# Optimization experiments

Measured on AMD Instinct MI355X. Metric: run time of the kernel, lower is better.

## Reference

```python
import jax, jax.numpy as jnp
import numpy as np

N, E, NODE_DIM, EDGE_DIM, H, L, G, C = 50000, 600000, 64, 16, 128, 3, 256, 2


def setup_inputs() -> dict:
    key = jax.random.key(0)
    ks = jax.random.split(key, 32)
    inp = {
        "x": jax.random.normal(ks[0], (N, NODE_DIM), jnp.float32),
        "edge_attr": jax.random.normal(ks[1], (E, EDGE_DIM), jnp.float32),
        "edge_index": jax.random.randint(ks[2], (2, E), 0, N, dtype=jnp.int64),
        "batch": jnp.sort(jax.random.randint(ks[3], (N,), 0, G, dtype=jnp.int64)),
    }
    def lin(k, fan_in, fan_out):
        b = 1.0 / np.sqrt(fan_in)
        return jax.random.uniform(k, (fan_in, fan_out), jnp.float32, -b, b)
    # node embedding
    inp["emb_W"] = lin(ks[4], NODE_DIM, H)
    inp["emb_b"] = jnp.zeros((H,), jnp.float32)
    # stacked per-layer MPNN params [L, ...]
    inp["msg_W1"] = jnp.stack([lin(jax.random.fold_in(ks[5], i), 2 * H + EDGE_DIM, H) for i in range(L)])
    inp["msg_b1"] = jnp.zeros((L, H), jnp.float32)
    inp["msg_W2"] = jnp.stack([lin(jax.random.fold_in(ks[6], i), H, H) for i in range(L)])
    inp["msg_b2"] = jnp.zeros((L, H), jnp.float32)
    inp["upd_W1"] = jnp.stack([lin(jax.random.fold_in(ks[7], i), 2 * H, H) for i in range(L)])
    inp["upd_b1"] = jnp.zeros((L, H), jnp.float32)
    inp["upd_W2"] = jnp.stack([lin(jax.random.fold_in(ks[8], i), H, H) for i in range(L)])
    inp["upd_b2"] = jnp.zeros((L, H), jnp.float32)
    # classifier (dropout is eval-mode identity)
    inp["cls_W1"] = lin(ks[9], 2 * H, H)
    inp["cls_b1"] = jnp.zeros((H,), jnp.float32)
    inp["cls_W2"] = lin(ks[10], H, H // 2)
    inp["cls_b2"] = jnp.zeros((H // 2,), jnp.float32)
    inp["cls_W3"] = lin(ks[11], H // 2, C)
    inp["cls_b3"] = jnp.zeros((C,), jnp.float32)
    return inp


def reference(x, edge_attr, emb_W, emb_b, msg_W1, msg_b1, msg_W2, msg_b2,
              upd_W1, upd_b1, upd_W2, upd_b2,
              cls_W1, cls_b1, cls_W2, cls_b2, cls_W3, cls_b3,
              edge_index, batch):
    src, dst = edge_index[0], edge_index[1]  # PyG: x_j = x[src], x_i = x[dst]
    h = x @ emb_W + emb_b  # [N, H]
    for l in range(L):
        x_i = h[dst]
        x_j = h[src]
        msg_in = jnp.concatenate([x_i, x_j, edge_attr], axis=1)  # [E, 2H+edge_dim]
        m = jax.nn.relu(msg_in @ msg_W1[l] + msg_b1[l]) @ msg_W2[l] + msg_b2[l]
        aggr = jax.ops.segment_sum(m, dst, num_segments=N)  # scatter-add to targets
        upd_in = jnp.concatenate([h, aggr], axis=1)  # [N, 2H]
        h = jax.nn.relu(upd_in @ upd_W1[l] + upd_b1[l]) @ upd_W2[l] + upd_b2[l]
        h = jax.nn.relu(h)
    # global mean / max pool over graphs
    counts = jax.ops.segment_sum(jnp.ones((N,), h.dtype), batch, num_segments=G)
    g_mean = jax.ops.segment_sum(h, batch, num_segments=G) / jnp.maximum(counts, 1.0)[:, None]
    g_max = jax.ops.segment_max(h, batch, num_segments=G)
    g_max = jnp.where(jnp.isfinite(g_max), g_max, 0.0)  # guard empty graphs
    rep = jnp.concatenate([g_mean, g_max], axis=1)  # [G, 2H]
    # classifier (dropout = identity in eval)
    z = jax.nn.relu(rep @ cls_W1 + cls_b1)
    z = jax.nn.relu(z @ cls_W2 + cls_b2)
    return z @ cls_W3 + cls_b3  # [G, C]
```

## Files before the change

### kernel.cpp

```cpp
#include <hip/hip_runtime.h>
#include <hip/hip_bf16.h>

#define HD 128
#define SCB 2048

typedef __attribute__((ext_vector_type(8))) short short8v;
typedef __attribute__((ext_vector_type(4))) float f32x4;
typedef unsigned short us;

__device__ __forceinline__ us f2bf(float f) {
    union { float f; unsigned u; } c; c.f = f;
    unsigned u = c.u;
    return (us)((u + 0x7fffu + ((u >> 16) & 1u)) >> 16);
}
__device__ __forceinline__ float bf2f(us b) {
    union { unsigned u; float f; } c; c.u = ((unsigned)b) << 16;
    return c.f;
}

__device__ __forceinline__ void gload16(const void* g, void* l) {
    __builtin_amdgcn_global_load_lds(
        (const __attribute__((address_space(1))) unsigned int*)g,
        (__attribute__((address_space(3))) unsigned int*)l,
        16, 0, 0);
}

template<int KSTEPS, int K1S, bool HASA2, bool RELU, bool DEGB, bool WF32, bool WBF>
__global__ __launch_bounds__(512) void k_mgemm(
    const us* __restrict__ A1h, const us* __restrict__ A1l,
    const us* __restrict__ A2h, const us* __restrict__ A2l,
    const us* __restrict__ Wth, const us* __restrict__ Wtl,
    const float* __restrict__ bias,
    const float* __restrict__ bdeg, const float* __restrict__ deg,
    float* __restrict__ Cf0, float* __restrict__ Cf1,
    us* __restrict__ Ch, us* __restrict__ Cl,
    int nrows)
{
    constexpr int K   = KSTEPS * 32;
    constexpr int CPR = K / 8;
    constexpr int ITER = (64 * CPR) / 512;
    __shared__ us As_h[64 * K];
    __shared__ us As_l[64 * K];

    const int tid  = threadIdx.x;
    const int wv   = tid >> 6;
    const int lane = tid & 63;
    const int r    = lane & 15;
    const int g    = lane >> 4;
    const int rb   = blockIdx.x * 64;
    const int col  = blockIdx.y * 128 + wv * 16 + r;

    short8v bh[KSTEPS], bl[KSTEPS];
    {
        size_t wbase = (size_t)col * K + (size_t)(g * 8);
#pragma unroll
        for (int s = 0; s < KSTEPS; ++s) {
            bh[s] = *(const short8v*)(Wth + wbase + s * 32);
            bl[s] = *(const short8v*)(Wtl + wbase + s * 32);
        }
    }

#pragma unroll
    for (int i = 0; i < ITER; ++i) {
        int f = tid + i * 512;
        int row = f / CPR, c = f % CPR;
        int grow = rb + row; if (grow >= nrows) grow = nrows - 1;
        int sb = (c * 16) ^ ((row & 7) << 4);
        const char *gh, *gl;
        if (!HASA2 || sb < K1S * 2) {
            gh = (const char*)A1h + (size_t)grow * (K1S * 2) + sb;
            gl = (const char*)A1l + (size_t)grow * (K1S * 2) + sb;
        } else {
            gh = (const char*)A2h + (size_t)grow * ((K - K1S) * 2) + (sb - K1S * 2);
            gl = (const char*)A2l + (size_t)grow * ((K - K1S) * 2) + (sb - K1S * 2);
        }
        gload16(gh, (char*)As_h + (size_t)f * 16);
        gload16(gl, (char*)As_l + (size_t)f * 16);
    }
    __syncthreads();

    f32x4 acc[4];
#pragma unroll
    for (int t = 0; t < 4; ++t) acc[t] = (f32x4){0.f, 0.f, 0.f, 0.f};

#pragma unroll
    for (int s = 0; s < KSTEPS; ++s) {
#pragma unroll
        for (int t = 0; t < 4; ++t) {
            int row = t * 16 + r;
            int boff = row * (K * 2) + (((s * 64) + g * 16) ^ ((row & 7) << 4));
            short8v ah = *(const short8v*)((const char*)As_h + boff);
            short8v al = *(const short8v*)((const char*)As_l + boff);
            acc[t] = __builtin_amdgcn_mfma_f32_16x16x32_bf16(ah, bh[s], acc[t], 0, 0, 0);
            acc[t] = __builtin_amdgcn_mfma_f32_16x16x32_bf16(al, bh[s], acc[t], 0, 0, 0);
            acc[t] = __builtin_amdgcn_mfma_f32_16x16x32_bf16(ah, bl[s], acc[t], 0, 0, 0);
        }
    }

    const float bb = (bias && col < 128) ? bias[col] : 0.f;
    const float bd = (DEGB && col < 128) ? bdeg[col] : 0.f;
    const int jc = col & 127;
#pragma unroll
    for (int t = 0; t < 4; ++t) {
#pragma unroll
        for (int i = 0; i < 4; ++i) {
            int row = rb + t * 16 + g * 4 + i;
            if (row >= nrows) continue;
            float v = acc[t][i] + bb;
            if (DEGB) v += deg[row] * bd;
            if (RELU) v = fmaxf(v, 0.f);
            size_t o = (size_t)row * HD + jc;
            if (WF32) (col < 128 ? Cf0 : Cf1)[o] = v;
            if (WBF) {
                us hh = f2bf(v);
                Ch[o] = hh;
                Cl[o] = f2bf(v - bf2f(hh));
            }
        }
    }
}

__global__ __launch_bounds__(512) void k_upd(
    const us* __restrict__ A1h, const us* __restrict__ A1l,
    const us* __restrict__ A2h, const us* __restrict__ A2l,
    const us* __restrict__ Wth, const us* __restrict__ Wtl,
    const float* __restrict__ b1,
    const float* __restrict__ bdeg, const float* __restrict__ deg,
    const us* __restrict__ W2th, const us* __restrict__ W2tl,
    const float* __restrict__ b2,
    us* __restrict__ out_h, us* __restrict__ out_l,
    int nrows)
{
    constexpr int K = 256;
    constexpr int CPR = K / 8;
    constexpr int ITER = (64 * CPR) / 512;
    __shared__ us As_h[64 * K];
    __shared__ us As_l[64 * K];

    const int tid  = threadIdx.x;
    const int wv   = tid >> 6;
    const int lane = tid & 63;
    const int r    = lane & 15;
    const int g    = lane >> 4;
    const int rb   = blockIdx.x * 64;
    const int col  = wv * 16 + r;

    short8v bh[8], bl[8];
    {
        size_t wbase = (size_t)col * K + (size_t)(g * 8);
#pragma unroll
        for (int s = 0; s < 8; ++s) {
            bh[s] = *(const short8v*)(Wth + wbase + s * 32);
            bl[s] = *(const short8v*)(Wtl + wbase + s * 32);
        }
    }

#pragma unroll
    for (int i = 0; i < ITER; ++i) {
        int f = tid + i * 512;
        int row = f / CPR, c = f % CPR;
        int grow = rb + row; if (grow >= nrows) grow = nrows - 1;
        int sb = (c * 16) ^ ((row & 7) << 4);
        const char *gh, *gl;
        if (sb < 256) {
            gh = (const char*)A1h + (size_t)grow * 256 + sb;
            gl = (const char*)A1l + (size_t)grow * 256 + sb;
        } else {
            gh = (const char*)A2h + (size_t)grow * 256 + (sb - 256);
            gl = (const char*)A2l + (size_t)grow * 256 + (sb - 256);
        }
        gload16(gh, (char*)As_h + (size_t)f * 16);
        gload16(gl, (char*)As_l + (size_t)f * 16);
    }
    __syncthreads();

    f32x4 acc[4];
#pragma unroll
    for (int t = 0; t < 4; ++t) acc[t] = (f32x4){0.f, 0.f, 0.f, 0.f};
#pragma unroll
    for (int s = 0; s < 8; ++s) {
#pragma unroll
        for (int t = 0; t < 4; ++t) {
            int row = t * 16 + r;
            int boff = row * (K * 2) + (((s * 64) + g * 16) ^ ((row & 7) << 4));
            short8v ah = *(const short8v*)((const char*)As_h + boff);
            short8v al = *(const short8v*)((const char*)As_l + boff);
            acc[t] = __builtin_amdgcn_mfma_f32_16x16x32_bf16(ah, bh[s], acc[t], 0, 0, 0);
            acc[t] = __builtin_amdgcn_mfma_f32_16x16x32_bf16(al, bh[s], acc[t], 0, 0, 0);
            acc[t] = __builtin_amdgcn_mfma_f32_16x16x32_bf16(ah, bl[s], acc[t], 0, 0, 0);
        }
    }
    __syncthreads();

    short8v b2h[4], b2l[4];
    {
        size_t wbase = (size_t)col * 128 + (size_t)(g * 8);
#pragma unroll
        for (int s = 0; s < 4; ++s) {
            b2h[s] = *(const short8v*)(W2th + wbase + s * 32);
            b2l[s] = *(const short8v*)(W2tl + wbase + s * 32);
        }
    }

    {
        const float bb = b1[col];
        const float bd = bdeg[col];
#pragma unroll
        for (int t = 0; t < 4; ++t) {
#pragma unroll
            for (int i = 0; i < 4; ++i) {
                int lrow = t * 16 + g * 4 + i;
                int grow = rb + lrow;
                float dg = (grow < nrows) ? deg[grow] : 0.f;
                float v = acc[t][i] + bb + dg * bd;
                v = fmaxf(v, 0.f);
                us uh = f2bf(v);
                us ul = f2bf(v - bf2f(uh));
                int byte = lrow * 256 + ((col * 2) ^ ((lrow & 7) << 4));
                *(us*)((char*)As_h + byte) = uh;
                *(us*)((char*)As_l + byte) = ul;
            }
        }
    }
    __syncthreads();

    f32x4 acc2[4];
#pragma unroll
    for (int t = 0; t < 4; ++t) acc2[t] = (f32x4){0.f, 0.f, 0.f, 0.f};
#pragma unroll
    for (int s = 0; s < 4; ++s) {
#pragma unroll
        for (int t = 0; t < 4; ++t) {
            int row = t * 16 + r;
            int boff = row * 256 + (((s * 64) + g * 16) ^ ((row & 7) << 4));
            short8v ah = *(const short8v*)((const char*)As_h + boff);
            short8v al = *(const short8v*)((const char*)As_l + boff);
            acc2[t] = __builtin_amdgcn_mfma_f32_16x16x32_bf16(ah, b2h[s], acc2[t], 0, 0, 0);
            acc2[t] = __builtin_amdgcn_mfma_f32_16x16x32_bf16(al, b2h[s], acc2[t], 0, 0, 0);
            acc2[t] = __builtin_amdgcn_mfma_f32_16x16x32_bf16(ah, b2l[s], acc2[t], 0, 0, 0);
        }
    }
    const float bb2 = b2[col];
#pragma unroll
    for (int t = 0; t < 4; ++t) {
#pragma unroll
        for (int i = 0; i < 4; ++i) {
            int row = rb + t * 16 + g * 4 + i;
            if (row >= nrows) continue;
            float v = fmaxf(acc2[t][i] + bb2, 0.f);
            size_t o = (size_t)row * HD + col;
            us hh = f2bf(v);
            out_h[o] = hh;
            out_l[o] = f2bf(v - bf2f(hh));
        }
    }
}

__global__ void k_cvtA(const float* __restrict__ src,
                       us* __restrict__ dh, us* __restrict__ dl, long n)
{
    long i = (long)blockIdx.x * blockDim.x + threadIdx.x;
    if (i >= n) return;
    float v = src[i];
    us h = f2bf(v);
    dh[i] = h;
    dl[i] = f2bf(v - bf2f(h));
}

__global__ void k_cvtW(const float* __restrict__ src, long sstride, int K,
                       us* __restrict__ dh, us* __restrict__ dl, long dstride)
{
    int l = blockIdx.y;
    int idx = blockIdx.x * 256 + threadIdx.x;
    if (idx >= K * 128) return;
    int k = idx >> 7, j = idx & 127;
    float v = src[(size_t)l * sstride + (size_t)k * 128 + j];
    us h = f2bf(v);
    size_t o = (size_t)l * dstride + (size_t)j * K + k;
    dh[o] = h;
    dl[o] = f2bf(v - bf2f(h));
}

__global__ void k_cvtW2(const float* __restrict__ srcA, long strideA,
                        const float* __restrict__ srcB, long strideB,
                        int K1s, int K,
                        us* __restrict__ dh, us* __restrict__ dl, long dstride)
{
    int l = blockIdx.y;
    int idx = blockIdx.x * 256 + threadIdx.x;
    if (idx >= K * 128) return;
    int k = idx >> 7, j = idx & 127;
    float v = (k < K1s)
        ? srcA[(size_t)l * strideA + (size_t)k * 128 + j]
        : srcB[(size_t)l * strideB + (size_t)(k - K1s) * 128 + j];
    us h = f2bf(v);
    size_t o = (size_t)l * dstride + (size_t)j * K + k;
    dh[o] = h;
    dl[o] = f2bf(v - bf2f(h));
}

__global__ void k_deghist(const int* __restrict__ dst, int* __restrict__ degi, int E,
                          const int* __restrict__ batch, int* __restrict__ gcnt, int N)
{
    int i = blockIdx.x * blockDim.x + threadIdx.x;
    if (i < E) atomicAdd(&degi[dst[i]], 1);
    if (i < N) atomicAdd(&gcnt[batch[i]], 1);
}

__global__ __launch_bounds__(256) void k_scan1(const int* __restrict__ degi,
                                               int* __restrict__ thrpre,
                                               int* __restrict__ bsum, int N)
{
    __shared__ int sc[256];
    const int t = threadIdx.x, b = blockIdx.x;
    int i0 = b * SCB + t * 8;
    int s = 0;
#pragma unroll
    for (int q = 0; q < 8; ++q) {
        int i = i0 + q;
        if (i < N) s += degi[i];
    }
    sc[t] = s;
    __syncthreads();
    for (int o = 1; o < 256; o <<= 1) {
        int v = (t >= o) ? sc[t - o] : 0;
        __syncthreads();
        sc[t] += v;
        __syncthreads();
    }
    thrpre[b * 256 + t] = sc[t] - s;
    if (t == 255) bsum[b] = sc[255];
}

__global__ void k_scan2(const int* __restrict__ bsum, int* __restrict__ boff, int nb)
{
    if (threadIdx.x == 0 && blockIdx.x == 0) {
        int run = 0;
        for (int b = 0; b < nb; ++b) { boff[b] = run; run += bsum[b]; }
    }
}

__global__ __launch_bounds__(256) void k_scan3(
    const int* __restrict__ degi, const int* __restrict__ thrpre,
    const int* __restrict__ boff,
    int* __restrict__ rowptr, int* __restrict__ cursor,
    float* __restrict__ degf, int N, int E)
{
    const int t = threadIdx.x, b = blockIdx.x;
    int run = boff[b] + thrpre[b * 256 + t];
    int i0 = b * SCB + t * 8;
#pragma unroll
    for (int q = 0; q < 8; ++q) {
        int i = i0 + q;
        if (i < N) {
            int d = degi[i];
            rowptr[i] = run;
            cursor[i] = run;
            degf[i] = (float)d;
            run += d;
        }
    }
    if (b == 0 && t == 0) rowptr[N] = E;
}

__global__ void k_scatter(const int* __restrict__ dst, const int* __restrict__ src,
                          int* __restrict__ cursor,
                          const float* __restrict__ ea,
                          int* __restrict__ csr_src, int* __restrict__ csr_eid,
                          float* __restrict__ ea_p, int E)
{
    int e = blockIdx.x * blockDim.x + threadIdx.x;
    if (e >= E) return;
    int d = dst[e];
    int pos = atomicAdd(&cursor[d], 1);
    csr_src[pos] = src[e];
    if (ea_p) {
        const float4* s4 = (const float4*)&ea[(size_t)e * 16];
        float4* d4 = (float4*)&ea_p[(size_t)pos * 16];
        d4[0] = s4[0]; d4[1] = s4[1]; d4[2] = s4[2]; d4[3] = s4[3];
    } else {
        csr_eid[pos] = e;
    }
}

__global__ __launch_bounds__(256) void k_foldW(
    const float* __restrict__ msg_W2, const float* __restrict__ upd_W1,
    float* __restrict__ fold)
{
    int l = blockIdx.x >> 3, rb = blockIdx.x & 7;
    const float* W2  = msg_W2 + (size_t)l * HD * HD;
    const float* U1b = upd_W1 + (size_t)l * 256 * HD + (size_t)HD * HD;
    float* Wout = fold + (size_t)l * HD * HD;
    int j = threadIdx.x & 127;
    int rh = threadIdx.x >> 7;
    int r0 = rb * 16 + rh * 8;
    float acc[8] = {0.f,0.f,0.f,0.f,0.f,0.f,0.f,0.f};
    for (int k = 0; k < HD; ++k) {
        float u = U1b[(size_t)k * HD + j];
#pragma unroll
        for (int rr = 0; rr < 8; ++rr)
            acc[rr] = fmaf(W2[(size_t)(r0 + rr) * HD + k], u, acc[rr]);
    }
#pragma unroll
    for (int rr = 0; rr < 8; ++rr)
        Wout[(size_t)(r0 + rr) * HD + j] = acc[rr];
}

__global__ __launch_bounds__(128) void k_foldb(
    const float* __restrict__ msg_b2, const float* __restrict__ upd_W1,
    float* __restrict__ bvec2)
{
    int l = blockIdx.x, j = threadIdx.x;
    const float* U1b = upd_W1 + (size_t)l * 256 * HD + (size_t)HD * HD;
    const float* b2 = msg_b2 + (size_t)l * HD;
    float acc = 0.f;
    for (int k = 0; k < HD; ++k) acc = fmaf(b2[k], U1b[(size_t)k * HD + j], acc);
    bvec2[(size_t)l * HD + j] = acc;
}

#define EB 16
template<bool PERM>
__global__ __launch_bounds__(256) void k_edge(
    const float* __restrict__ P, const float* __restrict__ Q,
    const float* __restrict__ EA,
    const int* __restrict__ rowptr,
    const int* __restrict__ csr_src, const int* __restrict__ csr_eid,
    const float* __restrict__ W1c,
    us* __restrict__ Sh, us* __restrict__ Sl, int N)
{
    const int lane = threadIdx.x & 63;
    const int node = __builtin_amdgcn_readfirstlane(blockIdx.x * 4 + (threadIdx.x >> 6));
    if (node >= N) return;
    float wA[16], wB[16];
#pragma unroll
    for (int k = 0; k < 16; ++k) {
        wA[k] = W1c[k * HD + lane];
        wB[k] = W1c[k * HD + 64 + lane];
    }
    const int beg = __builtin_amdgcn_readfirstlane(rowptr[node]);
    const int end = __builtin_amdgcn_readfirstlane(rowptr[node + 1]);
    const float pA = P[(size_t)node * HD + lane];
    const float pB = P[(size_t)node * HD + 64 + lane];
    float accA = 0.f, accB = 0.f;

    for (int i = beg; i < end; i += EB) {
        int myi = i + (lane & 15);
        myi = (myi < end) ? myi : (end - 1);
        int myidx = PERM ? myi : csr_eid[myi];
        int mysrc = csr_src[myi];
        int sv[EB], ei[EB];
#pragma unroll
        for (int r = 0; r < EB; ++r) {
            sv[r] = __builtin_amdgcn_readlane(mysrc, r);
            ei[r] = PERM ? 0 : __builtin_amdgcn_readlane(myidx, r);
        }
        float qA[EB], qB[EB];
#pragma unroll
        for (int r = 0; r < EB; ++r) {
            qA[r] = Q[(size_t)sv[r] * HD + lane];
            qB[r] = Q[(size_t)sv[r] * HD + 64 + lane];
        }
#pragma unroll
        for (int r = 0; r < EB; ++r) {
            int ii = i + r; ii = (ii < end) ? ii : (end - 1);
            const float4* Ev = PERM ? (const float4*)&EA[(size_t)ii * 16]
                                    : (const float4*)&EA[(size_t)ei[r] * 16];
            float4 v0 = Ev[0], v1 = Ev[1], v2 = Ev[2], v3 = Ev[3];
            float tA = pA + qA[r], tB = pB + qB[r];
            tA = fmaf(v0.x, wA[0],  tA); tB = fmaf(v0.x, wB[0],  tB);
            tA = fmaf(v0.y, wA[1],  tA); tB = fmaf(v0.y, wB[1],  tB);
            tA = fmaf(v0.z, wA[2],  tA); tB = fmaf(v0.z, wB[2],  tB);
            tA = fmaf(v0.w, wA[3],  tA); tB = fmaf(v0.w, wB[3],  tB);
            tA = fmaf(v1.x, wA[4],  tA); tB = fmaf(v1.x, wB[4],  tB);
            tA = fmaf(v1.y, wA[5],  tA); tB = fmaf(v1.y, wB[5],  tB);
            tA = fmaf(v1.z, wA[6],  tA); tB = fmaf(v1.z, wB[6],  tB);
            tA = fmaf(v1.w, wA[7],  tA); tB = fmaf(v1.w, wB[7],  tB);
            tA = fmaf(v2.x, wA[8],  tA); tB = fmaf(v2.x, wB[8],  tB);
            tA = fmaf(v2.y, wA[9],  tA); tB = fmaf(v2.y, wB[9],  tB);
            tA = fmaf(v2.z, wA[10], tA); tB = fmaf(v2.z, wB[10], tB);
            tA = fmaf(v2.w, wA[11], tA); tB = fmaf(v2.w, wB[11], tB);
            tA = fmaf(v3.x, wA[12], tA); tB = fmaf(v3.x, wB[12], tB);
            tA = fmaf(v3.y, wA[13], tA); tB = fmaf(v3.y, wB[13], tB);
            tA = fmaf(v3.z, wA[14], tA); tB = fmaf(v3.z, wB[14], tB);
            tA = fmaf(v3.w, wA[15], tA); tB = fmaf(v3.w, wB[15], tB);
            bool ok = (i + r) < end;
            accA += ok ? fmaxf(tA, 0.f) : 0.f;
            accB += ok ? fmaxf(tB, 0.f) : 0.f;
        }
    }
    size_t oA = (size_t)node * HD + lane;
    size_t oB = oA + 64;
    us hA = f2bf(accA);
    us hB = f2bf(accB);
    Sh[oA] = hA; Sl[oA] = f2bf(accA - bf2f(hA));
    Sh[oB] = hB; Sl[oB] = f2bf(accB - bf2f(hB));
}

__global__ __launch_bounds__(256) void k_pool2(
    const us* __restrict__ hh, const us* __restrict__ hl,
    const int* __restrict__ batch,
    float* __restrict__ gsum, unsigned int* __restrict__ gmax, int N)
{
    int nchunk = (N + gridDim.x - 1) / gridDim.x;
    int n0 = blockIdx.x * nchunk;
    int n1 = n0 + nchunk; if (n1 > N) n1 = N;
    int j = threadIdx.x & 127;
    int half = threadIdx.x >> 7;
    float s = 0.f, m = 0.f; int gcur = -1;
    for (int n = n0 + half; n < n1; n += 2) {
        int g = batch[n];
        if (g != gcur) {
            if (gcur >= 0) {
                atomicAdd(&gsum[(size_t)gcur * HD + j], s);
                atomicMax(&gmax[(size_t)gcur * HD + j], __float_as_uint(m));
            }
            gcur = g; s = 0.f; m = 0.f;
        }
        size_t o = (size_t)n * HD + j;
        float v = bf2f(hh[o]) + bf2f(hl[o]);
        s += v; m = fmaxf(m, v);
    }
    if (gcur >= 0) {
        atomicAdd(&gsum[(size_t)gcur * HD + j], s);
        atomicMax(&gmax[(size_t)gcur * HD + j], __float_as_uint(m));
    }
}

__global__ __launch_bounds__(128) void k_cls(
    const float* __restrict__ gsum, const float* __restrict__ gmax,
    const int* __restrict__ gcnt,
    const float* __restrict__ W1, const float* __restrict__ b1,
    const float* __restrict__ W2, const float* __restrict__ b2,
    const float* __restrict__ W3, const float* __restrict__ b3,
    float* __restrict__ out)
{
    __shared__ float rep[256];
    __shared__ float z1[128];
    __shared__ float z2[64];
    const int g = blockIdx.x;
    const int j = threadIdx.x;
    float cntf = (float)gcnt[g];
    rep[j]       = gsum[(size_t)g * HD + j] / fmaxf(cntf, 1.f);
    rep[128 + j] = gmax[(size_t)g * HD + j];
    __syncthreads();
    float a = 0.f;
    for (int k = 0; k < 256; ++k) a = fmaf(rep[k], W1[(size_t)k * 128 + j], a);
    z1[j] = fmaxf(a + b1[j], 0.f);
    __syncthreads();
    if (j < 64) {
        float b = 0.f;
        for (int k = 0; k < 128; ++k) b = fmaf(z1[k], W2[(size_t)k * 64 + j], b);
        z2[j] = fmaxf(b + b2[j], 0.f);
    }
    __syncthreads();
    if (j < 2) {
        float c = 0.f;
        for (int k = 0; k < 64; ++k) c = fmaf(z2[k], W3[(size_t)k * 2 + j], c);
        out[(size_t)g * 2 + j] = c + b3[j];
    }
}

extern "C" void kernel_launch(void* const* d_in, const int* in_sizes, int n_in,
                              void* d_out, int out_size, void* d_ws, size_t ws_size,
                              hipStream_t stream) {
    const float* x      = (const float*)d_in[0];
    const float* ea     = (const float*)d_in[1];
    const int*   ei     = (const int*)d_in[2];
    const int*   batch  = (const int*)d_in[3];
    const float* emb_W  = (const float*)d_in[4];
    const float* emb_b  = (const float*)d_in[5];
    const float* msg_W1 = (const float*)d_in[6];
    const float* msg_b1 = (const float*)d_in[7];
    const float* msg_W2 = (const float*)d_in[8];
    const float* msg_b2 = (const float*)d_in[9];
    const float* upd_W1 = (const float*)d_in[10];
    const float* upd_b1 = (const float*)d_in[11];
    const float* upd_W2 = (const float*)d_in[12];
    const float* upd_b2 = (const float*)d_in[13];
    const float* cW1 = (const float*)d_in[14];
    const float* cb1 = (const float*)d_in[15];
    const float* cW2 = (const float*)d_in[16];
    const float* cb2 = (const float*)d_in[17];
    const float* cW3 = (const float*)d_in[18];
    const float* cb3 = (const float*)d_in[19];

    const int N = in_sizes[0] / 64;
    const int E = in_sizes[1] / 16;
    const int G = 256, L = 3;
    const int* src = ei;
    const int* dst = ei + E;
    const int nb = (N + SCB - 1) / SCB;

    char* w = (char*)d_ws;
    size_t off = 0;
    auto alloc = [&](size_t bytes) -> void* {
        void* p = w + off;
        off += (bytes + 255) & ~(size_t)255;
        return p;
    };
    float* Pb  = (float*)alloc((size_t)N * HD * 4);
    float* Qb  = (float*)alloc((size_t)N * HD * 4);
    us* S_h = (us*)alloc((size_t)N * HD * 2);
    us* S_l = (us*)alloc((size_t)N * HD * 2);
    us* h_h = (us*)alloc((size_t)N * HD * 2);
    us* h_l = (us*)alloc((size_t)N * HD * 2);
    us* x_h = S_h;
    us* x_l = S_l;
    float* fold  = (float*)alloc((size_t)L * HD * HD * 4);
    float* bvec2 = (float*)alloc((size_t)L * HD * 4);
    us* embt_h = (us*)alloc((size_t)128 * 64 * 2);
    us* embt_l = (us*)alloc((size_t)128 * 64 * 2);
    us* WPQt_h = (us*)alloc((size_t)L * 256 * 128 * 2);
    us* WPQt_l = (us*)alloc((size_t)L * 256 * 128 * 2);
    us* Wcbt_h = (us*)alloc((size_t)L * 128 * 256 * 2);
    us* Wcbt_l = (us*)alloc((size_t)L * 128 * 256 * 2);
    us* U2t_h  = (us*)alloc((size_t)L * 128 * 128 * 2);
    us* U2t_l  = (us*)alloc((size_t)L * 128 * 128 * 2);
    int*   degi   = (int*)alloc((size_t)N * 4);
    float* degf   = (float*)alloc((size_t)N * 4);
    int*   rowptr = (int*)alloc((size_t)(N + 1) * 4);
    int*   cursor = (int*)alloc((size_t)N * 4);
    int*   thrpre = (int*)alloc((size_t)nb * 256 * 4);
    int*   bsum   = (int*)alloc((size_t)(nb + 1) * 4);
    int*   boff   = (int*)alloc((size_t)(nb + 1) * 4);
    int*   gcnt   = (int*)alloc(256 * 4);
    float* gsum   = (float*)alloc((size_t)G * HD * 4);
    float* gmax   = (float*)alloc((size_t)G * HD * 4);
    int*   csr_src = (int*)alloc((size_t)E * 4);
    int*   csr_eid = (int*)alloc((size_t)E * 4);
    float* ea_p = nullptr;
    if (ws_size && off + (size_t)E * 16 * 4 + 256 <= ws_size)
        ea_p = (float*)alloc((size_t)E * 16 * 4);
    (void)n_in; (void)out_size;

    hipMemsetAsync(degi, 0, (size_t)N * 4, stream);
    hipMemsetAsync(gcnt, 0, 256 * 4, stream);
    hipMemsetAsync(gsum, 0, (size_t)G * HD * 4, stream);
    hipMemsetAsync(gmax, 0, (size_t)G * HD * 4, stream);

    int mEN = (E > N ? E : N);
    k_deghist<<<(mEN + 255) / 256, 256, 0, stream>>>(dst, degi, E, batch, gcnt, N);
    k_scan1<<<nb, 256, 0, stream>>>(degi, thrpre, bsum, N);
    k_scan2<<<1, 64, 0, stream>>>(bsum, boff, nb);
    k_scan3<<<nb, 256, 0, stream>>>(degi, thrpre, boff, rowptr, cursor, degf, N, E);
    k_scatter<<<(E + 255) / 256, 256, 0, stream>>>(dst, src, cursor, ea,
                                                   csr_src, csr_eid, ea_p, E);

    k_foldW<<<L * 8, 256, 0, stream>>>(msg_W2, upd_W1, fold);
    k_foldb<<<L, 128, 0, stream>>>(msg_b2, upd_W1, bvec2);

    k_cvtA<<<(int)(((long)N * 64 + 255) / 256), 256, 0, stream>>>(x, x_h, x_l, (long)N * 64);
    k_cvtW<<<dim3(32, 1), 256, 0, stream>>>(emb_W, 0, 64, embt_h, embt_l, 0);
    k_cvtW<<<dim3(64, L), 256, 0, stream>>>(msg_W1, 272 * 128, 128,
                                            WPQt_h, WPQt_l, 256 * 128);
    k_cvtW<<<dim3(64, L), 256, 0, stream>>>(msg_W1 + 128 * 128, 272 * 128, 128,
                                            WPQt_h + 128 * 128, WPQt_l + 128 * 128,
                                            256 * 128);
    k_cvtW2<<<dim3(128, L), 256, 0, stream>>>(upd_W1, 256 * 128, fold, 128 * 128,
                                              128, 256, Wcbt_h, Wcbt_l, 128 * 256);
    k_cvtW<<<dim3(64, L), 256, 0, stream>>>(upd_W2, 128 * 128, 128,
                                            U2t_h, U2t_l, 128 * 128);

    const int gb = (N + 63) / 64;
    k_mgemm<2, 64, false, false, false, false, true><<<dim3(gb, 1), 512, 0, stream>>>(
        x_h, x_l, nullptr, nullptr, embt_h, embt_l,
        emb_b, nullptr, nullptr, nullptr, nullptr, h_h, h_l, N);

    for (int l = 0; l < L; ++l) {
        const float* W1 = msg_W1 + (size_t)l * 272 * HD;
        k_mgemm<4, 128, false, false, false, true, false><<<dim3(gb, 2), 512, 0, stream>>>(
            h_h, h_l, nullptr, nullptr,
            WPQt_h + (size_t)l * 256 * 128, WPQt_l + (size_t)l * 256 * 128,
            msg_b1 + (size_t)l * HD, nullptr, nullptr, Pb, Qb, nullptr, nullptr, N);
        if (ea_p)
            k_edge<true><<<(N + 3) / 4, 256, 0, stream>>>(Pb, Qb, ea_p, rowptr,
                                                          csr_src, nullptr,
                                                          W1 + 256 * HD, S_h, S_l, N);
        else
            k_edge<false><<<(N + 3) / 4, 256, 0, stream>>>(Pb, Qb, ea, rowptr,
                                                           csr_src, csr_eid,
                                                           W1 + 256 * HD, S_h, S_l, N);
        k_upd<<<gb, 512, 0, stream>>>(
            h_h, h_l, S_h, S_l,
            Wcbt_h + (size_t)l * 128 * 256, Wcbt_l + (size_t)l * 128 * 256,
            upd_b1 + (size_t)l * HD, bvec2 + (size_t)l * HD, degf,
            U2t_h + (size_t)l * 128 * 128, U2t_l + (size_t)l * 128 * 128,
            upd_b2 + (size_t)l * HD,
            h_h, h_l, N);
    }

    k_pool2<<<1024, 256, 0, stream>>>(h_h, h_l, batch, gsum, (unsigned int*)gmax, N);
    k_cls<<<G, 128, 0, stream>>>(gsum, gmax, gcnt, cW1, cb1, cW2, cb2, cW3, cb3,
                                 (float*)d_out);
}
```

Before: 685.5 us.

## Fuse per-layer P/Q projection GEMM into embedding and update kernels

The standalone per-layer GEMM that computes the P and Q node projections is removed. That projection now runs inside the embedding kernel for layer 0 and inside the update kernel for the following layer. The freshly computed h tile is written back to shared memory and immediately multiplied by the W_P/W_Q weights, so h is not re-read from global memory and launches are saved. In exchange, the fused kernels use more registers for the extra weight fragments and accumulators, which may reduce occupancy.

```diff
diff --git a/kernel.cpp b/kernel.cpp
--- a/kernel.cpp
+++ b/kernel.cpp
@@ -25,22 +25,17 @@
         16, 0, 0);
 }
 
-template<int KSTEPS, int K1S, bool HASA2, bool RELU, bool DEGB, bool WF32, bool WBF>
-__global__ __launch_bounds__(512) void k_mgemm(
-    const us* __restrict__ A1h, const us* __restrict__ A1l,
-    const us* __restrict__ A2h, const us* __restrict__ A2l,
-    const us* __restrict__ Wth, const us* __restrict__ Wtl,
-    const float* __restrict__ bias,
-    const float* __restrict__ bdeg, const float* __restrict__ deg,
-    float* __restrict__ Cf0, float* __restrict__ Cf1,
-    us* __restrict__ Ch, us* __restrict__ Cl,
-    int nrows)
-{
-    constexpr int K   = KSTEPS * 32;
-    constexpr int CPR = K / 8;
-    constexpr int ITER = (64 * CPR) / 512;
-    __shared__ us As_h[64 * K];
-    __shared__ us As_l[64 * K];
+__global__ __launch_bounds__(512) void k_embpq(
+    const us* __restrict__ xh, const us* __restrict__ xl,
+    const us* __restrict__ embth, const us* __restrict__ embtl,
+    const float* __restrict__ emb_b,
+    const us* __restrict__ wpqh, const us* __restrict__ wpql,
+    const float* __restrict__ b1msg,
+    us* __restrict__ out_h, us* __restrict__ out_l,
+    float* __restrict__ Pb, float* __restrict__ Qb, int nrows)
+{
+    __shared__ us As_h[8192];
+    __shared__ us As_l[8192];
 
     const int tid  = threadIdx.x;
     const int wv   = tid >> 6;
@@ -48,47 +43,37 @@
     const int r    = lane & 15;
     const int g    = lane >> 4;
     const int rb   = blockIdx.x * 64;
-    const int col  = blockIdx.y * 128 + wv * 16 + r;
-
-    short8v bh[KSTEPS], bl[KSTEPS];
-    {
-        size_t wbase = (size_t)col * K + (size_t)(g * 8);
-#pragma unroll
-        for (int s = 0; s < KSTEPS; ++s) {
-            bh[s] = *(const short8v*)(Wth + wbase + s * 32);
-            bl[s] = *(const short8v*)(Wtl + wbase + s * 32);
-        }
-    }
-
-#pragma unroll
-    for (int i = 0; i < ITER; ++i) {
-        int f = tid + i * 512;
-        int row = f / CPR, c = f % CPR;
+    const int col  = wv * 16 + r;
+
+    short8v bh[2], bl[2];
+    {
+        size_t wbase = (size_t)col * 64 + (size_t)(g * 8);
+#pragma unroll
+        for (int s = 0; s < 2; ++s) {
+            bh[s] = *(const short8v*)(embth + wbase + s * 32);
+            bl[s] = *(const short8v*)(embtl + wbase + s * 32);
+        }
+    }
+
+    {
+        int f = tid;
+        int row = f >> 3, c = f & 7;
         int grow = rb + row; if (grow >= nrows) grow = nrows - 1;
         int sb = (c * 16) ^ ((row & 7) << 4);
-        const char *gh, *gl;
-        if (!HASA2 || sb < K1S * 2) {
-            gh = (const char*)A1h + (size_t)grow * (K1S * 2) + sb;
-            gl = (const char*)A1l + (size_t)grow * (K1S * 2) + sb;
-        } else {
-            gh = (const char*)A2h + (size_t)grow * ((K - K1S) * 2) + (sb - K1S * 2);
-            gl = (const char*)A2l + (size_t)grow * ((K - K1S) * 2) + (sb - K1S * 2);
-        }
-        gload16(gh, (char*)As_h + (size_t)f * 16);
-        gload16(gl, (char*)As_l + (size_t)f * 16);
+        gload16((const char*)xh + (size_t)grow * 128 + sb, (char*)As_h + (size_t)f * 16);
+        gload16((const char*)xl + (size_t)grow * 128 + sb, (char*)As_l + (size_t)f * 16);
     }
     __syncthreads();
 
     f32x4 acc[4];
 #pragma unroll
     for (int t = 0; t < 4; ++t) acc[t] = (f32x4){0.f, 0.f, 0.f, 0.f};
-
-#pragma unroll
-    for (int s = 0; s < KSTEPS; ++s) {
+#pragma unroll
+    for (int s = 0; s < 2; ++s) {
 #pragma unroll
         for (int t = 0; t < 4; ++t) {
             int row = t * 16 + r;
-            int boff = row * (K * 2) + (((s * 64) + g * 16) ^ ((row & 7) << 4));
+            int boff = row * 128 + (((s * 64) + g * 16) ^ ((row & 7) << 4));
             short8v ah = *(const short8v*)((const char*)As_h + boff);
             short8v al = *(const short8v*)((const char*)As_l + boff);
             acc[t] = __builtin_amdgcn_mfma_f32_16x16x32_bf16(ah, bh[s], acc[t], 0, 0, 0);
@@ -96,31 +81,84 @@
             acc[t] = __builtin_amdgcn_mfma_f32_16x16x32_bf16(ah, bl[s], acc[t], 0, 0, 0);
         }
     }
-
-    const float bb = (bias && col < 128) ? bias[col] : 0.f;
-    const float bd = (DEGB && col < 128) ? bdeg[col] : 0.f;
-    const int jc = col & 127;
+    __syncthreads();
+
+    {
+        const float bbE = emb_b[col];
+#pragma unroll
+        for (int t = 0; t < 4; ++t) {
+#pragma unroll
+            for (int i = 0; i < 4; ++i) {
+                int lrow = t * 16 + g * 4 + i;
+                int grow = rb + lrow;
+                float v = acc[t][i] + bbE;
+                us hh = f2bf(v);
+                us hl2 = f2bf(v - bf2f(hh));
+                if (grow < nrows) {
+                    size_t o = (size_t)grow * HD + col;
+                    out_h[o] = hh; out_l[o] = hl2;
+                }
+                int byte = lrow * 256 + ((col * 2) ^ ((lrow & 7) << 4));
+                *(us*)((char*)As_h + byte) = hh;
+                *(us*)((char*)As_l + byte) = hl2;
+            }
+        }
+    }
+    __syncthreads();
+
+    short8v bPh[4], bPl[4], bQh[4], bQl[4];
+    {
+        size_t baseP = (size_t)col * 128 + (size_t)(g * 8);
+        size_t baseQ = (size_t)(col + 128) * 128 + (size_t)(g * 8);
+#pragma unroll
+        for (int s = 0; s < 4; ++s) {
+            bPh[s] = *(const short8v*)(wpqh + baseP + s * 32);
+            bPl[s] = *(const short8v*)(wpql + baseP + s * 32);
+            bQh[s] = *(const short8v*)(wpqh + baseQ + s * 32);
+            bQl[s] = *(const short8v*)(wpql + baseQ + s * 32);
+        }
+    }
+
+    f32x4 accP[4], accQ[4];
 #pragma unroll
     for (int t = 0; t < 4; ++t) {
-#pragma unroll
-        for (int i = 0; i < 4; ++i) {
-            int row = rb + t * 16 + g * 4 + i;
-            if (row >= nrows) continue;
-            float v = acc[t][i] + bb;
-            if (DEGB) v += deg[row] * bd;
-            if (RELU) v = fmaxf(v, 0.f);
-            size_t o = (size_t)row * HD + jc;
-            if (WF32) (col < 128 ? Cf0 : Cf1)[o] = v;
-            if (WBF) {
-                us hh = f2bf(v);
-                Ch[o] = hh;
-                Cl[o] = f2bf(v - bf2f(hh));
+        accP[t] = (f32x4){0.f, 0.f, 0.f, 0.f};
+        accQ[t] = (f32x4){0.f, 0.f, 0.f, 0.f};
+    }
+#pragma unroll
+    for (int s = 0; s < 4; ++s) {
+#pragma unroll
+        for (int t = 0; t < 4; ++t) {
+            int row = t * 16 + r;
+            int boff = row * 256 + (((s * 64) + g * 16) ^ ((row & 7) << 4));
+            short8v ah = *(const short8v*)((const char*)As_h + boff);
+            short8v al = *(const short8v*)((const char*)As_l + boff);
+            accP[t] = __builtin_amdgcn_mfma_f32_16x16x32_bf16(ah, bPh[s], accP[t], 0, 0, 0);
+            accP[t] = __builtin_amdgcn_mfma_f32_16x16x32_bf16(al, bPh[s], accP[t], 0, 0, 0);
+            accP[t] = __builtin_amdgcn_mfma_f32_16x16x32_bf16(ah, bPl[s], accP[t], 0, 0, 0);
+            accQ[t] = __builtin_amdgcn_mfma_f32_16x16x32_bf16(ah, bQh[s], accQ[t], 0, 0, 0);
+            accQ[t] = __builtin_amdgcn_mfma_f32_16x16x32_bf16(al, bQh[s], accQ[t], 0, 0, 0);
+            accQ[t] = __builtin_amdgcn_mfma_f32_16x16x32_bf16(ah, bQl[s], accQ[t], 0, 0, 0);
+        }
+    }
+    {
+        const float bbP = b1msg[col];
+#pragma unroll
+        for (int t = 0; t < 4; ++t) {
+#pragma unroll
+            for (int i = 0; i < 4; ++i) {
+                int row = rb + t * 16 + g * 4 + i;
+                if (row >= nrows) continue;
+                size_t o = (size_t)row * HD + col;
+                Pb[o] = accP[t][i] + bbP;
+                Qb[o] = accQ[t][i];
             }
         }
     }
 }
 
-__global__ __launch_bounds__(512) void k_upd(
+template<bool DOPQ>
+__global__ __launch_bounds__(512) void k_updpq(
     const us* __restrict__ A1h, const us* __restrict__ A1l,
     const us* __restrict__ A2h, const us* __restrict__ A2l,
     const us* __restrict__ Wth, const us* __restrict__ Wtl,
@@ -128,7 +166,10 @@
     const float* __restrict__ bdeg, const float* __restrict__ deg,
     const us* __restrict__ W2th, const us* __restrict__ W2tl,
     const float* __restrict__ b2,
+    const us* __restrict__ wpqh, const us* __restrict__ wpql,
+    const float* __restrict__ b1msg,
     us* __restrict__ out_h, us* __restrict__ out_l,
+    float* __restrict__ Pb, float* __restrict__ Qb,
     int nrows)
 {
     constexpr int K = 256;
@@ -240,18 +281,94 @@
             acc2[t] = __builtin_amdgcn_mfma_f32_16x16x32_bf16(ah, b2l[s], acc2[t], 0, 0, 0);
         }
     }
-    const float bb2 = b2[col];
+    if (!DOPQ) {
+        const float bb2 = b2[col];
+#pragma unroll
+        for (int t = 0; t < 4; ++t) {
+#pragma unroll
+            for (int i = 0; i < 4; ++i) {
+                int row = rb + t * 16 + g * 4 + i;
+                if (row >= nrows) continue;
+                float v = fmaxf(acc2[t][i] + bb2, 0.f);
+                size_t o = (size_t)row * HD + col;
+                us hh = f2bf(v);
+                out_h[o] = hh;
+                out_l[o] = f2bf(v - bf2f(hh));
+            }
+        }
+        return;
+    }
+
+    __syncthreads();
+    {
+        const float bb2 = b2[col];
+#pragma unroll
+        for (int t = 0; t < 4; ++t) {
+#pragma unroll
+            for (int i = 0; i < 4; ++i) {
+                int lrow = t * 16 + g * 4 + i;
+                int grow = rb + lrow;
+                float v = fmaxf(acc2[t][i] + bb2, 0.f);
+                us hh = f2bf(v);
+                us hl2 = f2bf(v - bf2f(hh));
+                if (grow < nrows) {
+                    size_t o = (size_t)grow * HD + col;
+                    out_h[o] = hh; out_l[o] = hl2;
+                }
+                int byte = lrow * 256 + ((col * 2) ^ ((lrow & 7) << 4));
+                *(us*)((char*)As_h + byte) = hh;
+                *(us*)((char*)As_l + byte) = hl2;
+            }
+        }
+    }
+    __syncthreads();
+
+    short8v bPh[4], bPl[4], bQh[4], bQl[4];
+    {
+        size_t baseP = (size_t)col * 128 + (size_t)(g * 8);
+        size_t baseQ = (size_t)(col + 128) * 128 + (size_t)(g * 8);
+#pragma unroll
+        for (int s = 0; s < 4; ++s) {
+            bPh[s] = *(const short8v*)(wpqh + baseP + s * 32);
+            bPl[s] = *(const short8v*)(wpql + baseP + s * 32);
+            bQh[s] = *(const short8v*)(wpqh + baseQ + s * 32);
+            bQl[s] = *(const short8v*)(wpql + baseQ + s * 32);
+        }
+    }
+    f32x4 accP[4], accQ[4];
 #pragma unroll
     for (int t = 0; t < 4; ++t) {
-#pragma unroll
-        for (int i = 0; i < 4; ++i) {
-            int row = rb + t * 16 + g * 4 + i;
-            if (row >= nrows) continue;
-            float v = fmaxf(acc2[t][i] + bb2, 0.f);
-            size_t o = (size_t)row * HD + col;
-            us hh = f2bf(v);
-            out_h[o] = hh;
-            out_l[o] = f2bf(v - bf2f(hh));
+        accP[t] = (f32x4){0.f, 0.f, 0.f, 0.f};
+        accQ[t] = (f32x4){0.f, 0.f, 0.f, 0.f};
+    }
+#pragma unroll
+    for (int s = 0; s < 4; ++s) {
+#pragma unroll
+        for (int t = 0; t < 4; ++t) {
+            int row = t * 16 + r;
+            int boff = row * 256 + (((s * 64) + g * 16) ^ ((row & 7) << 4));
+            short8v ah = *(const short8v*)((const char*)As_h + boff);
+            short8v al = *(const short8v*)((const char*)As_l + boff);
+            accP[t] = __builtin_amdgcn_mfma_f32_16x16x32_bf16(ah, bPh[s], accP[t], 0, 0, 0);
+            accP[t] = __builtin_amdgcn_mfma_f32_16x16x32_bf16(al, bPh[s], accP[t], 0, 0, 0);
+            accP[t] = __builtin_amdgcn_mfma_f32_16x16x32_bf16(ah, bPl[s], accP[t], 0, 0, 0);
+            accQ[t] = __builtin_amdgcn_mfma_f32_16x16x32_bf16(ah, bQh[s], accQ[t], 0, 0, 0);
+            accQ[t] = __builtin_amdgcn_mfma_f32_16x16x32_bf16(al, bQh[s], accQ[t], 0, 0, 0);
+            accQ[t] = __builtin_amdgcn_mfma_f32_16x16x32_bf16(ah, bQl[s], accQ[t], 0, 0, 0);
+        }
+    }
+    {
+        const float bbP = b1msg[col];
+#pragma unroll
+        for (int t = 0; t < 4; ++t) {
+#pragma unroll
+            for (int i = 0; i < 4; ++i) {
+                int row = rb + t * 16 + g * 4 + i;
+                if (row >= nrows) continue;
+                size_t o = (size_t)row * HD + col;
+                Pb[o] = accP[t][i] + bbP;
+                Qb[o] = accQ[t][i];
+            }
         }
     }
 }
@@ -662,16 +779,12 @@
                                             U2t_h, U2t_l, 128 * 128);
 
     const int gb = (N + 63) / 64;
-    k_mgemm<2, 64, false, false, false, false, true><<<dim3(gb, 1), 512, 0, stream>>>(
-        x_h, x_l, nullptr, nullptr, embt_h, embt_l,
-        emb_b, nullptr, nullptr, nullptr, nullptr, h_h, h_l, N);
+    k_embpq<<<gb, 512, 0, stream>>>(x_h, x_l, embt_h, embt_l, emb_b,
+                                    WPQt_h, WPQt_l, msg_b1,
+                                    h_h, h_l, Pb, Qb, N);
 
     for (int l = 0; l < L; ++l) {
         const float* W1 = msg_W1 + (size_t)l * 272 * HD;
-        k_mgemm<4, 128, false, false, false, true, false><<<dim3(gb, 2), 512, 0, stream>>>(
-            h_h, h_l, nullptr, nullptr,
-            WPQt_h + (size_t)l * 256 * 128, WPQt_l + (size_t)l * 256 * 128,
-            msg_b1 + (size_t)l * HD, nullptr, nullptr, Pb, Qb, nullptr, nullptr, N);
         if (ea_p)
             k_edge<true><<<(N + 3) / 4, 256, 0, stream>>>(Pb, Qb, ea_p, rowptr,
                                                           csr_src, nullptr,
@@ -680,13 +793,26 @@
             k_edge<false><<<(N + 3) / 4, 256, 0, stream>>>(Pb, Qb, ea, rowptr,
                                                            csr_src, csr_eid,
                                                            W1 + 256 * HD, S_h, S_l, N);
-        k_upd<<<gb, 512, 0, stream>>>(
-            h_h, h_l, S_h, S_l,
-            Wcbt_h + (size_t)l * 128 * 256, Wcbt_l + (size_t)l * 128 * 256,
-            upd_b1 + (size_t)l * HD, bvec2 + (size_t)l * HD, degf,
-            U2t_h + (size_t)l * 128 * 128, U2t_l + (size_t)l * 128 * 128,
-            upd_b2 + (size_t)l * HD,
-            h_h, h_l, N);
+        if (l < L - 1)
+            k_updpq<true><<<gb, 512, 0, stream>>>(
+                h_h, h_l, S_h, S_l,
+                Wcbt_h + (size_t)l * 128 * 256, Wcbt_l + (size_t)l * 128 * 256,
+                upd_b1 + (size_t)l * HD, bvec2 + (size_t)l * HD, degf,
+                U2t_h + (size_t)l * 128 * 128, U2t_l + (size_t)l * 128 * 128,
+                upd_b2 + (size_t)l * HD,
+                WPQt_h + (size_t)(l + 1) * 256 * 128,
+                WPQt_l + (size_t)(l + 1) * 256 * 128,
+                msg_b1 + (size_t)(l + 1) * HD,
+                h_h, h_l, Pb, Qb, N);
+        else
+            k_updpq<false><<<gb, 512, 0, stream>>>(
+                h_h, h_l, S_h, S_l,
+                Wcbt_h + (size_t)l * 128 * 256, Wcbt_l + (size_t)l * 128 * 256,
+                upd_b1 + (size_t)l * HD, bvec2 + (size_t)l * HD, degf,
+                U2t_h + (size_t)l * 128 * 128, U2t_l + (size_t)l * 128 * 128,
+                upd_b2 + (size_t)l * HD,
+                nullptr, nullptr, nullptr,
+                h_h, h_l, nullptr, nullptr, N);
     }
 
     k_pool2<<<1024, 256, 0, stream>>>(h_h, h_l, batch, gsum, (unsigned int*)gmax, N);
```

Result: faster. 666.7 us (-2.7%).
